# Optimization experiments

Hardware: AMD Instinct MI355X
Metric: run time of the kernel (lower is better)

The kernel has to match this reference:

```python
import jax, jax.numpy as jnp
import numpy as np

ALPHA_MGD = 2e-05
NOISE_SIGMA = 8.0
NOISE_VAR = NOISE_SIGMA ** 2  # 64.0


def _conv2d(x, w, b, pad):
    # x: [N,C,H,W], w: [O,I,kh,kw]
    y = jax.lax.conv_general_dilated(
        x, w, window_strides=(1, 1), padding=[(pad, pad), (pad, pad)],
        dimension_numbers=("NCHW", "OIHW", "NCHW"))
    return y + b[None, :, None, None]


def setup_inputs() -> dict:
    key = jax.random.key(0)
    ks = jax.random.split(key, 8)
    N, Cs, Ct, H, W = 8, 128, 256, 64, 64
    return {
        "preds_S": jax.random.normal(ks[0], (N, Cs, H, W), jnp.float32),
        "preds_T": jax.random.normal(ks[1], (N, Ct, H, W), jnp.float32),
        "W_align": jax.random.normal(ks[2], (Ct, Cs, 1, 1), jnp.float32) * 0.05,
        "b_align": jnp.zeros((Ct,), jnp.float32),
        "W_gen1": jax.random.normal(ks[3], (Ct, Ct, 3, 3), jnp.float32) * 0.02,
        "b_gen1": jnp.zeros((Ct,), jnp.float32),
        "W_gen2": jax.random.normal(ks[4], (Ct, Ct, 3, 3), jnp.float32) * 0.02,
        "b_gen2": jnp.zeros((Ct,), jnp.float32),
    }


def reference(preds_S, preds_T, W_align, b_align, W_gen1, b_gen1, W_gen2, b_gen2):
    # align student channels to teacher channels (1x1 conv)
    s = _conv2d(preds_S, W_align, b_align, pad=0)
    N, C, H, W = preds_T.shape
    # deterministic checkerboard mask: tile([[0,1],[1,0]]) cropped to HxW -> (h+w) % 2
    hh = jnp.arange(H)[:, None]
    ww = jnp.arange(W)[None, :]
    mat = ((hh + ww) % 2).astype(s.dtype)  # [H,W]
    masked_fea = s * mat  # broadcast over [N,C,H,W]
    # generation network: conv3x3 -> relu -> conv3x3
    new_fea = _conv2d(jax.nn.relu(_conv2d(masked_fea, W_gen1, b_gen1, pad=1)), W_gen2, b_gen2, pad=1)
    # bmc_loss_md(pred=preds_T, target=new_fea, noise_var=64):
    # logits[i,j] = MVN(pred_i, noise_var*I).log_prob(target_j); the normalization
    # constant is class-independent and cancels in cross-entropy, keep the quadratic term.
    p = preds_T.reshape(N, -1)   # [N, D], D = C*H*W
    t = new_fea.reshape(N, -1)   # [N, D]
    # pairwise squared L2 via ||p||^2 + ||t||^2 - 2 p.t  (avoids NxNxD blow-up)
    sq = (jnp.sum(p * p, axis=1)[:, None]
          + jnp.sum(t * t, axis=1)[None, :]
          - 2.0 * (p @ t.T))  # [N, N]
    logits = -0.5 * sq / NOISE_VAR
    # cross_entropy(logits, arange(N)) = mean_i (logsumexp_j logits[i,j] - logits[i,i])
    ce = jnp.mean(jax.nn.logsumexp(logits, axis=1) - jnp.diagonal(logits))
    loss = ce * (2.0 * NOISE_VAR) / N
    return loss * ALPHA_MGD
```

## Files before the change

kernel.cpp:

```cpp
#include <hip/hip_runtime.h>

typedef unsigned short u16;
typedef short short8 __attribute__((ext_vector_type(8)));
typedef unsigned short ushort8 __attribute__((ext_vector_type(8)));
typedef float floatx16 __attribute__((ext_vector_type(16)));

#define PLANE8   34848
#define NSTRIDE  1115136

__device__ __forceinline__ u16 f2b(float f) {
  unsigned u = __builtin_bit_cast(unsigned, f);
  return (u16)((u + 0x7FFFu + ((u >> 16) & 1u)) >> 16);
}
__device__ __forceinline__ float b2f(u16 b) {
  return __builtin_bit_cast(float, ((unsigned)b) << 16);
}

typedef const __attribute__((address_space(1))) unsigned int* gptr_t;
typedef __attribute__((address_space(3))) unsigned int* sptr_t;

__global__ __launch_bounds__(256) void kprep(
    const float* __restrict__ Wg1, u16* __restrict__ Wsw1,
    const float* __restrict__ Wg2, u16* __restrict__ Wsw2,
    const float* __restrict__ Wa,  u16* __restrict__ Wb,
    const float* __restrict__ pS,  u16* __restrict__ T,
    u16* __restrict__ masked, u16* __restrict__ t1)
{
  __shared__ u16 Ls[64 * 136];
  int b = blockIdx.x, t = threadIdx.x;

  if (b < 576) {
    const float* W = (b < 288) ? Wg1 : Wg2;
    u16* D = (b < 288) ? Wsw1 : Wsw2;
    int bb = (b < 288) ? b : b - 288;
    int cid = bb * 256 + t;
    int d = cid % 1152, ctcg = cid / 1152;
    int ct = ctcg & 3, cg = ctcg >> 2;
    int colow = d & 31, cihalf = (d >> 5) & 1, sc = (d >> 6) & 1, tap = d >> 7;
    int co = ct * 64 + sc * 32 + colow;
    short8 v;
    #pragma unroll
    for (int jj = 0; jj < 8; ++jj) {
      int ci = cg * 16 + cihalf * 8 + jj;
      v[jj] = (short)f2b(W[((size_t)(co * 256 + ci)) * 9 + tap]);
    }
    *(short8*)&D[(size_t)cid * 8] = v;
  } else if (b < 592) {
    int v = (b - 576) * 256 + t;
    int colow = v & 31, hfb = (v >> 5) & 1, cog = (v >> 6) & 7, k = v >> 9;
    int co = cog * 32 + colow;
    int ci0 = k * 16 + hfb * 8;
    float4 f0 = *(const float4*)(Wa + (size_t)co * 128 + ci0);
    float4 f1 = *(const float4*)(Wa + (size_t)co * 128 + ci0 + 4);
    short8 o;
    o[0] = (short)f2b(f0.x); o[1] = (short)f2b(f0.y);
    o[2] = (short)f2b(f0.z); o[3] = (short)f2b(f0.w);
    o[4] = (short)f2b(f1.x); o[5] = (short)f2b(f1.y);
    o[6] = (short)f2b(f1.z); o[7] = (short)f2b(f1.w);
    *(short8*)&Wb[(size_t)v * 8] = o;
  } else if (b < 1104) {
    int bb = b - 592;
    int n = bb >> 6, pt = bb & 63, pix0 = pt * 64;
    int ci = t >> 1, ph = t & 1;
    const float* src = pS + ((size_t)n * 128 + ci) * 4096 + pix0 + ph * 32;
    #pragma unroll
    for (int i = 0; i < 8; ++i) {
      float4 v4 = *(const float4*)(src + i * 4);
      int pix = ph * 32 + i * 4;
      Ls[(pix + 0) * 136 + ci] = f2b(v4.x);
      Ls[(pix + 1) * 136 + ci] = f2b(v4.y);
      Ls[(pix + 2) * 136 + ci] = f2b(v4.z);
      Ls[(pix + 3) * 136 + ci] = f2b(v4.w);
    }
    __syncthreads();
    int p = t >> 2, q = t & 3;
    const u16* row = Ls + p * 136 + q * 32;
    u16* dst = T + ((size_t)n * 4096 + pix0 + p) * 128 + q * 32;
    #pragma unroll
    for (int k2 = 0; k2 < 4; ++k2)
      *(ushort8*)(dst + k2 * 8) = *(const ushort8*)(row + k2 * 8);
  } else {
    int p = b - 1104;
    u16* base = ((p >> 8) ? t1 : masked);
    int q = p & 255;
    base += (size_t)(q >> 5) * NSTRIDE + (size_t)(q & 31) * PLANE8;
    short8 z;
    #pragma unroll
    for (int jj = 0; jj < 8; ++jj) z[jj] = 0;
    #pragma unroll
    for (int pass = 0; pass < 2; ++pass) {
      int seg = t + pass * 256;
      if (seg < 264) {
        int off;
        if (seg < 66)       off = seg * 8;
        else if (seg < 132) off = (65 * 66 + (seg - 66)) * 8;
        else if (seg < 198) off = ((seg - 132) * 66) * 8;
        else                off = ((seg - 198) * 66 + 65) * 8;
        *(short8*)(base + off) = z;
      }
    }
  }
}

__global__ __launch_bounds__(256) void k1m(const u16* __restrict__ T,
    const u16* __restrict__ Wb, const float* __restrict__ ba,
    u16* __restrict__ mk)
{
  __shared__ __align__(16) u16 Wl[32768];
  int b = blockIdx.x;
  int n = b >> 5, pt = b & 31;
  int t = threadIdx.x, wid = t >> 6, lane = t & 63;
  int ml = lane & 31, hf = lane >> 5;

  #pragma unroll
  for (int kk = 0; kk < 16; ++kk) {
    int chunk = kk * 256 + t;
    __builtin_amdgcn_global_load_lds((gptr_t)(const void*)(Wb + (size_t)chunk * 8),
                                     (sptr_t)(void*)(Wl + chunk * 8), 16, 0, 0);
  }

  const u16* Tn = T + (size_t)n * 524288;
  const u16* ap[4];
  #pragma unroll
  for (int g = 0; g < 4; ++g)
    ap[g] = Tn + (size_t)(pt * 128 + g * 32 + ml) * 128 + hf * 8;

  floatx16 acc[2][4];
  #pragma unroll
  for (int q = 0; q < 2; ++q)
    #pragma unroll
    for (int g = 0; g < 4; ++g)
      #pragma unroll
      for (int i = 0; i < 16; ++i) acc[q][g][i] = 0.f;

  __syncthreads();

  const short8* WlV = (const short8*)Wl;
  int cogb = wid * 2;

  short8 a0[4], a1[4];
  #pragma unroll
  for (int g = 0; g < 4; ++g) a0[g] = *(const short8*)(ap[g]);

#define K1M_STEP(K, CUR, NXT, LAST)                                           \
  {                                                                           \
    if (!(LAST)) {                                                            \
      _Pragma("unroll")                                                       \
      for (int g = 0; g < 4; ++g)                                             \
        NXT[g] = *(const short8*)(ap[g] + ((K) + 1) * 16);                    \
    }                                                                         \
    short8 w0 = WlV[((K) * 8 + cogb) * 64 + lane];                            \
    short8 w1 = WlV[((K) * 8 + cogb + 1) * 64 + lane];                        \
    _Pragma("unroll")                                                         \
    for (int g = 0; g < 4; ++g) {                                             \
      acc[0][g] = __builtin_amdgcn_mfma_f32_32x32x16_bf16(CUR[g], w0, acc[0][g], 0, 0, 0); \
      acc[1][g] = __builtin_amdgcn_mfma_f32_32x32x16_bf16(CUR[g], w1, acc[1][g], 0, 0, 0); \
    }                                                                         \
  }
  K1M_STEP(0, a0, a1, 0)
  K1M_STEP(1, a1, a0, 0)
  K1M_STEP(2, a0, a1, 0)
  K1M_STEP(3, a1, a0, 0)
  K1M_STEP(4, a0, a1, 0)
  K1M_STEP(5, a1, a0, 0)
  K1M_STEP(6, a0, a1, 0)
  K1M_STEP(7, a1, a0, 1)
#undef K1M_STEP

  int co0 = cogb * 32 + ml, co1 = co0 + 32;
  float b0 = ba[co0], b1 = ba[co1];
  u16* base0 = mk + (size_t)n * NSTRIDE + (size_t)(co0 >> 3) * PLANE8 + (co0 & 7);
  u16* base1 = mk + (size_t)n * NSTRIDE + (size_t)(co1 >> 3) * PLANE8 + (co1 & 7);
  #pragma unroll
  for (int g = 0; g < 4; ++g)
    #pragma unroll
    for (int reg = 0; reg < 16; ++reg) {
      int m = (reg & 3) + 8 * (reg >> 2) + 4 * hf;
      int pix = pt * 128 + g * 32 + m;
      int h = pix >> 6, w = pix & 63;
      float msk = (float)((h + w) & 1);
      int off = ((h + 1) * 66 + (w + 1)) * 8;
      base0[off] = f2b((acc[0][g][reg] + b0) * msk);
      base1[off] = f2b((acc[1][g][reg] + b1) * msk);
    }
}

template <int MODE>
__global__ __launch_bounds__(512) void kconv(
    const u16* __restrict__ IN, const u16* __restrict__ WS,
    const float* __restrict__ bg, u16* __restrict__ OUT)
{
  __shared__ __align__(16) u16 L[40960];
  u16* LinA = L;
  u16* LwA  = L + 11264;
  u16* LinB = L + 20480;
  u16* LwB  = L + 31744;

  int b = blockIdx.x;
  int rt = b & 7, ct = (b >> 3) & 3, n = b >> 5;
  int h0 = rt * 8;
  int t = threadIdx.x;
  int wid = t >> 6, lane = t & 63;
  int hf = lane >> 5, ml = lane & 31;

  const u16* inb = IN + (size_t)n * NSTRIDE;
  const u16* wg  = WS + (size_t)ct * 1152 * 8;

  floatx16 acc[2][2];
  #pragma unroll
  for (int s = 0; s < 2; ++s)
    #pragma unroll
    for (int q = 0; q < 2; ++q)
      #pragma unroll
      for (int i = 0; i < 16; ++i) acc[s][q][i] = 0.f;

  auto STAGE = [&](int cg, u16* LinD, u16* LwD) {
    #pragma unroll
    for (int k = 0; k < 3; ++k) {
      int sidx = 8 * k + wid;
      if (sidx < 18) {
        const u16* src = wg + (size_t)cg * 36864 + (size_t)(sidx * 64 + lane) * 8;
        __builtin_amdgcn_global_load_lds((gptr_t)(const void*)src,
                                         (sptr_t)(void*)(LwD + sidx * 512), 16, 0, 0);
      }
    }
    #pragma unroll
    for (int k = 0; k < 3; ++k) {
      int seg = 8 * k + wid;
      if (seg < 22) {
        int half = seg >= 11 ? 1 : 0;
        int s = seg - half * 11;
        const u16* src = inb + (size_t)cg * 69696 + half * PLANE8
                         + (size_t)(h0 * 66 + s * 64 + lane) * 8;
        __builtin_amdgcn_global_load_lds((gptr_t)(const void*)src,
                                         (sptr_t)(void*)(LinD + (half * 704 + s * 64) * 8),
                                         16, 0, 0);
      }
    }
  };

  auto COMPUTE = [&](const u16* LinS, const u16* LwS) {
    const short8* LinV = (const short8*)LinS;
    const short8* LwV  = (const short8*)LwS;
    #pragma unroll
    for (int dr = 0; dr < 3; ++dr) {
      int r0 = hf * 704 + (wid + dr) * 66;
      #pragma unroll
      for (int dc = 0; dc < 3; ++dc) {
        int tap = dr * 3 + dc;
        short8 w0 = LwV[tap * 128 + lane];
        short8 w1 = LwV[tap * 128 + 64 + lane];
        short8 i0 = LinV[r0 + ml + dc];
        short8 i1 = LinV[r0 + 32 + ml + dc];
        acc[0][0] = __builtin_amdgcn_mfma_f32_32x32x16_bf16(i0, w0, acc[0][0], 0, 0, 0);
        acc[0][1] = __builtin_amdgcn_mfma_f32_32x32x16_bf16(i0, w1, acc[0][1], 0, 0, 0);
        acc[1][0] = __builtin_amdgcn_mfma_f32_32x32x16_bf16(i1, w0, acc[1][0], 0, 0, 0);
        acc[1][1] = __builtin_amdgcn_mfma_f32_32x32x16_bf16(i1, w1, acc[1][1], 0, 0, 0);
      }
    }
  };

  STAGE(0, LinA, LwA);
  __syncthreads();
  for (int cg = 0; cg < 16; cg += 2) {
    STAGE(cg + 1, LinB, LwB);
    COMPUTE(LinA, LwA);
    __syncthreads();
    if (cg + 2 < 16) STAGE(cg + 2, LinA, LwA);
    COMPUTE(LinB, LwB);
    __syncthreads();
  }

  float bias0 = bg[ct * 64 + ml];
  float bias1 = bg[ct * 64 + 32 + ml];

  if (MODE == 0) {
    u16* ob = OUT + (size_t)n * NSTRIDE;
    int co0 = ct * 64 + ml, co1 = co0 + 32;
    int cb0 = ((co0 >> 4) * 2 + ((co0 >> 3) & 1)) * PLANE8 + (co0 & 7);
    int cb1 = ((co1 >> 4) * 2 + ((co1 >> 3) & 1)) * PLANE8 + (co1 & 7);
    int rowoff = (h0 + wid + 1) * 66 + 1;
    #pragma unroll
    for (int reg = 0; reg < 16; ++reg) {
      int m = (reg & 3) + 8 * (reg >> 2) + 4 * hf;
      float v;
      v = acc[0][0][reg] + bias0; v = fmaxf(v, 0.f); ob[cb0 + (rowoff + m) * 8] = f2b(v);
      v = acc[0][1][reg] + bias1; v = fmaxf(v, 0.f); ob[cb1 + (rowoff + m) * 8] = f2b(v);
      v = acc[1][0][reg] + bias0; v = fmaxf(v, 0.f); ob[cb0 + (rowoff + 32 + m) * 8] = f2b(v);
      v = acc[1][1][reg] + bias1; v = fmaxf(v, 0.f); ob[cb1 + (rowoff + 32 + m) * 8] = f2b(v);
    }
  } else {
    u16* plane = L + wid * 4352;
    #pragma unroll
    for (int reg = 0; reg < 16; ++reg) {
      int m = (reg & 3) + 8 * (reg >> 2) + 4 * hf;
      plane[ml * 68 + m]              = f2b(acc[0][0][reg] + bias0);
      plane[(32 + ml) * 68 + m]       = f2b(acc[0][1][reg] + bias1);
      plane[ml * 68 + 32 + m]         = f2b(acc[1][0][reg] + bias0);
      plane[(32 + ml) * 68 + 32 + m]  = f2b(acc[1][1][reg] + bias1);
    }
    const u16* row = plane + lane * 68;
    __align__(16) u16 tmp[64];
    #pragma unroll
    for (int k2 = 0; k2 < 16; ++k2)
      *(ushort4*)(tmp + k2 * 4) = *(const ushort4*)(row + k2 * 4);
    u16* gdst = OUT + (size_t)n * 1048576 + (size_t)(ct * 64 + lane) * 4096
                + (h0 + wid) * 64;
    #pragma unroll
    for (int k2 = 0; k2 < 8; ++k2)
      *(ushort8*)(gdst + k2 * 8) = *(const ushort8*)(tmp + k2 * 8);
  }
}

__global__ __launch_bounds__(256) void kbmc(const u16* __restrict__ t2,
    const float* __restrict__ pT, float* __restrict__ part)
{
  int t = threadIdx.x, lane = t & 63, role = t >> 6;
  int ih = role >> 1, nh = role & 1;
  int bid = blockIdx.x;

  float pt[4][4], pp[4], tt[4];
  #pragma unroll
  for (int i = 0; i < 4; ++i) {
    pp[i] = 0.f; tt[i] = 0.f;
    #pragma unroll
    for (int j = 0; j < 4; ++j) pt[i][j] = 0.f;
  }

  const float* pb = pT + ((size_t)ih * 4) * 1048576;
  const u16*   tb = t2 + ((size_t)nh * 4) * 1048576;

  for (int k = 0; k < 8; ++k) {
    size_t d0 = ((size_t)(bid * 512 + k * 64 + lane)) * 4;
    float4 p[4], tf[4];
    #pragma unroll
    for (int i = 0; i < 4; ++i)
      p[i] = *(const float4*)(pb + (size_t)i * 1048576 + d0);
    #pragma unroll
    for (int j = 0; j < 4; ++j) {
      ushort4 tv = *(const ushort4*)(tb + (size_t)j * 1048576 + d0);
      tf[j] = make_float4(b2f(tv.x), b2f(tv.y), b2f(tv.z), b2f(tv.w));
    }
    if (nh == 0) {
      #pragma unroll
      for (int i = 0; i < 4; ++i)
        pp[i] += p[i].x * p[i].x + p[i].y * p[i].y + p[i].z * p[i].z + p[i].w * p[i].w;
    }
    if (ih == 0) {
      #pragma unroll
      for (int j = 0; j < 4; ++j)
        tt[j] += tf[j].x * tf[j].x + tf[j].y * tf[j].y + tf[j].z * tf[j].z + tf[j].w * tf[j].w;
    }
    #pragma unroll
    for (int i = 0; i < 4; ++i)
      #pragma unroll
      for (int j = 0; j < 4; ++j)
        pt[i][j] += p[i].x * tf[j].x + p[i].y * tf[j].y
                  + p[i].z * tf[j].z + p[i].w * tf[j].w;
  }

  #pragma unroll
  for (int m = 1; m < 64; m <<= 1) {
    #pragma unroll
    for (int i = 0; i < 4; ++i) {
      pp[i] += __shfl_xor(pp[i], m);
      tt[i] += __shfl_xor(tt[i], m);
      #pragma unroll
      for (int j = 0; j < 4; ++j) pt[i][j] += __shfl_xor(pt[i][j], m);
    }
  }
  if (lane == 0) {
    #pragma unroll
    for (int i = 0; i < 4; ++i)
      #pragma unroll
      for (int j = 0; j < 4; ++j)
        part[(size_t)(16 + (ih * 4 + i) * 8 + (nh * 4 + j)) * 512 + bid] = pt[i][j];
    if (nh == 0) {
      #pragma unroll
      for (int i = 0; i < 4; ++i) part[(size_t)(ih * 4 + i) * 512 + bid] = pp[i];
    }
    if (ih == 0) {
      #pragma unroll
      for (int j = 0; j < 4; ++j) part[(size_t)(8 + nh * 4 + j) * 512 + bid] = tt[j];
    }
  }
}

__global__ __launch_bounds__(256) void kred(const float* __restrict__ part,
                                            float* __restrict__ accums)
{
  __shared__ float r4[4];
  int s = blockIdx.x, t = threadIdx.x, lane = t & 63, wid = t >> 6;
  float v = part[(size_t)s * 512 + t] + part[(size_t)s * 512 + 256 + t];
  #pragma unroll
  for (int m = 1; m < 64; m <<= 1) v += __shfl_xor(v, m);
  if (lane == 0) r4[wid] = v;
  __syncthreads();
  if (t == 0) accums[s] = r4[0] + r4[1] + r4[2] + r4[3];
}

__global__ void k4_final(const float* __restrict__ accums, float* __restrict__ out)
{
  int t = threadIdx.x;
  int i = t >> 3, j = t & 7;
  double pp = accums[i];
  double tt = accums[8 + j];
  double pt = accums[16 + i * 8 + j];
  double logit = -0.5 * (pp + tt - 2.0 * pt) / 64.0;
  double m = logit;
  #pragma unroll
  for (int s = 1; s < 8; s <<= 1) {
    double o = __shfl_xor(m, s);
    m = o > m ? o : m;
  }
  double e = exp(logit - m);
  #pragma unroll
  for (int s = 1; s < 8; s <<= 1) e += __shfl_xor(e, s);
  double lse = m + log(e);
  double term = (j == i) ? (lse - logit) : 0.0;
  #pragma unroll
  for (int s = 1; s < 64; s <<= 1) term += __shfl_xor(term, s);
  if (t == 0) {
    double ce = term / 8.0;
    out[0] = (float)(ce * (2.0 * 64.0) / 8.0 * 2e-05);
  }
}

extern "C" void kernel_launch(void* const* d_in, const int* in_sizes, int n_in,
                              void* d_out, int out_size, void* d_ws, size_t ws_size,
                              hipStream_t stream)
{
  const float* preds_S = (const float*)d_in[0];
  const float* preds_T = (const float*)d_in[1];
  const float* W_align = (const float*)d_in[2];
  const float* b_align = (const float*)d_in[3];
  const float* W_gen1  = (const float*)d_in[4];
  const float* b_gen1  = (const float*)d_in[5];
  const float* W_gen2  = (const float*)d_in[6];
  const float* b_gen2  = (const float*)d_in[7];
  float* out = (float*)d_out;

  char* wsb = (char*)d_ws;
  u16* masked = (u16*)wsb;
  u16* t1     = (u16*)(wsb + 17842176);
  u16* t2p    = (u16*)(wsb + 35684352);
  u16* T      = t2p;
  u16* Wsw1   = (u16*)(wsb + 52461568);
  u16* Wsw2   = (u16*)(wsb + 53641216);
  float* part   = (float*)(wsb + 54820864);
  float* accums = (float*)(wsb + 55017472);
  u16* Wb     = (u16*)(wsb + 55017856);

  kprep<<<1616, 256, 0, stream>>>(W_gen1, Wsw1, W_gen2, Wsw2, W_align, Wb,
                                  preds_S, T, masked, t1);
  k1m<<<256, 256, 0, stream>>>(T, Wb, b_align, masked);
  kconv<0><<<256, 512, 0, stream>>>(masked, Wsw1, b_gen1, t1);
  kconv<1><<<256, 512, 0, stream>>>(t1, Wsw2, b_gen2, t2p);
  kbmc<<<512, 256, 0, stream>>>(t2p, preds_T, part);
  kred<<<80, 256, 0, stream>>>(part, accums);
  k4_final<<<1, 64, 0, stream>>>(accums, out);
}
```

Baseline: 208.0 us.

## Store checkerboard-masked features compactly and skip zero taps in first 3x3 conv

The aligned student features are now stored in a compacted layout that holds only the nonzero checkerboard pixels, roughly halving the masked buffer. A new conv kernel (kconvs) for the first generator conv exploits the parity structure: for each output parity only the taps that hit nonzero inputs are computed (4 or 5 of the 9). This removes about half of the MFMA work and input traffic for that conv. In exchange it adds parity-dependent indexing and a new padding layout that must exactly match the zeroing in kprep and the writes in k1m.

```diff
diff --git a/kernel.cpp b/kernel.cpp
--- a/kernel.cpp
+++ b/kernel.cpp
@@ -5,6 +5,8 @@
 typedef unsigned short ushort8 __attribute__((ext_vector_type(8)));
 typedef float floatx16 __attribute__((ext_vector_type(16)));
 
+#define PLANE8C  17952
+#define NSTRIDEC 574464
 #define PLANE8   34848
 #define NSTRIDE  1115136
 
@@ -24,7 +26,7 @@
     const float* __restrict__ Wg2, u16* __restrict__ Wsw2,
     const float* __restrict__ Wa,  u16* __restrict__ Wb,
     const float* __restrict__ pS,  u16* __restrict__ T,
-    u16* __restrict__ masked, u16* __restrict__ t1)
+    u16* __restrict__ maskedC, u16* __restrict__ t1)
 {
   __shared__ u16 Ls[64 * 136];
   int b = blockIdx.x, t = threadIdx.x;
@@ -79,11 +81,23 @@
     #pragma unroll
     for (int k2 = 0; k2 < 4; ++k2)
       *(ushort8*)(dst + k2 * 8) = *(const ushort8*)(row + k2 * 8);
+  } else if (b < 1360) {
+    int p = b - 1104;
+    u16* base = maskedC + (size_t)(p >> 5) * NSTRIDEC + (size_t)(p & 31) * PLANE8C;
+    short8 z;
+    #pragma unroll
+    for (int jj = 0; jj < 8; ++jj) z[jj] = 0;
+    if (t < 200) {
+      int off;
+      if (t < 34)       off = t * 8;
+      else if (t < 68)  off = (65 * 34 + (t - 34)) * 8;
+      else if (t < 134) off = ((t - 68) * 34) * 8;
+      else              off = ((t - 134) * 34 + 33) * 8;
+      *(short8*)(base + off) = z;
+    }
   } else {
-    int p = b - 1104;
-    u16* base = ((p >> 8) ? t1 : masked);
-    int q = p & 255;
-    base += (size_t)(q >> 5) * NSTRIDE + (size_t)(q & 31) * PLANE8;
+    int p = b - 1360;
+    u16* base = t1 + (size_t)(p >> 5) * NSTRIDE + (size_t)(p & 31) * PLANE8;
     short8 z;
     #pragma unroll
     for (int jj = 0; jj < 8; ++jj) z[jj] = 0;
@@ -169,8 +183,8 @@
 
   int co0 = cogb * 32 + ml, co1 = co0 + 32;
   float b0 = ba[co0], b1 = ba[co1];
-  u16* base0 = mk + (size_t)n * NSTRIDE + (size_t)(co0 >> 3) * PLANE8 + (co0 & 7);
-  u16* base1 = mk + (size_t)n * NSTRIDE + (size_t)(co1 >> 3) * PLANE8 + (co1 & 7);
+  u16* base0 = mk + (size_t)n * NSTRIDEC + (size_t)(co0 >> 3) * PLANE8C + (co0 & 7);
+  u16* base1 = mk + (size_t)n * NSTRIDEC + (size_t)(co1 >> 3) * PLANE8C + (co1 & 7);
   #pragma unroll
   for (int g = 0; g < 4; ++g)
     #pragma unroll
@@ -178,11 +192,132 @@
       int m = (reg & 3) + 8 * (reg >> 2) + 4 * hf;
       int pix = pt * 128 + g * 32 + m;
       int h = pix >> 6, w = pix & 63;
-      float msk = (float)((h + w) & 1);
-      int off = ((h + 1) * 66 + (w + 1)) * 8;
-      base0[off] = f2b((acc[0][g][reg] + b0) * msk);
-      base1[off] = f2b((acc[1][g][reg] + b1) * msk);
-    }
+      if (((h + w) & 1) == 1) {
+        int j = (w - ((h + 1) & 1)) >> 1;
+        int off = ((h + 1) * 34 + 1 + j) * 8;
+        base0[off] = f2b(acc[0][g][reg] + b0);
+        base1[off] = f2b(acc[1][g][reg] + b1);
+      }
+    }
+}
+
+__global__ __launch_bounds__(512) void kconvs(
+    const u16* __restrict__ IN, const u16* __restrict__ WS,
+    const float* __restrict__ bg, u16* __restrict__ OUT)
+{
+  __shared__ __align__(16) u16 L[30720];
+  u16* LinA = L;
+  u16* LwA  = L + 6144;
+  u16* LinB = L + 15360;
+  u16* LwB  = L + 21504;
+
+  int b = blockIdx.x;
+  int rt = b & 7, ct = (b >> 3) & 3, n = b >> 5;
+  int h0 = rt * 8;
+  int t = threadIdx.x;
+  int wid = t >> 6, lane = t & 63;
+  int hf = lane >> 5, ml = lane & 31;
+  int e = wid & 1;
+
+  const u16* inb = IN + (size_t)n * NSTRIDEC;
+  const u16* wg  = WS + (size_t)ct * 1152 * 8;
+
+  floatx16 acc[2][2];
+  #pragma unroll
+  for (int p = 0; p < 2; ++p)
+    #pragma unroll
+    for (int q = 0; q < 2; ++q)
+      #pragma unroll
+      for (int i = 0; i < 16; ++i) acc[p][q][i] = 0.f;
+
+  auto STAGE = [&](int cg, u16* LinD, u16* LwD) {
+    #pragma unroll
+    for (int k = 0; k < 4; ++k) {
+      int seg = wid + 8 * k;
+      if (seg < 18) {
+        const u16* src = wg + (size_t)cg * 36864 + (size_t)(seg * 64 + lane) * 8;
+        __builtin_amdgcn_global_load_lds((gptr_t)(const void*)src,
+                                         (sptr_t)(void*)(LwD + seg * 512), 16, 0, 0);
+      } else if (seg < 30) {
+        int ii = seg - 18;
+        int hh = ii >= 6 ? 1 : 0;
+        int s = ii - hh * 6;
+        const u16* src = inb + (size_t)cg * (2 * PLANE8C) + (size_t)hh * PLANE8C
+                         + (size_t)(h0 * 34 + s * 64 + lane) * 8;
+        __builtin_amdgcn_global_load_lds((gptr_t)(const void*)src,
+                                         (sptr_t)(void*)(LinD + (hh * 384 + s * 64) * 8),
+                                         16, 0, 0);
+      }
+    }
+  };
+
+  auto COMPUTE = [&](const u16* LinS, const u16* LwS) {
+    const short8* LinV = (const short8*)LinS;
+    const short8* LwV  = (const short8*)LwS;
+    int rA = hf * 384 + wid * 34 + 1 + ml;
+    int rS = rA + 34;
+    int rB = rA + 68;
+    short8 iA0 = LinV[rA];
+    short8 iS0 = LinV[rS];
+    short8 iB0 = LinV[rB];
+    short8 iSm = LinV[rS + e - 1];
+    short8 iSp = LinV[rS + e];
+    short8 iAm = LinV[rA - e];
+    short8 iAp = LinV[rA + 1 - e];
+    short8 iBm = LinV[rB - e];
+    short8 iBp = LinV[rB + 1 - e];
+    #pragma unroll
+    for (int q = 0; q < 2; ++q) {
+      short8 w0 = LwV[0 * 128 + q * 64 + lane];
+      short8 w1 = LwV[1 * 128 + q * 64 + lane];
+      short8 w2 = LwV[2 * 128 + q * 64 + lane];
+      short8 w3 = LwV[3 * 128 + q * 64 + lane];
+      short8 w4 = LwV[4 * 128 + q * 64 + lane];
+      short8 w5 = LwV[5 * 128 + q * 64 + lane];
+      short8 w6 = LwV[6 * 128 + q * 64 + lane];
+      short8 w7 = LwV[7 * 128 + q * 64 + lane];
+      short8 w8 = LwV[8 * 128 + q * 64 + lane];
+      acc[0][q] = __builtin_amdgcn_mfma_f32_32x32x16_bf16(iA0, w1, acc[0][q], 0, 0, 0);
+      acc[0][q] = __builtin_amdgcn_mfma_f32_32x32x16_bf16(iSm, w3, acc[0][q], 0, 0, 0);
+      acc[0][q] = __builtin_amdgcn_mfma_f32_32x32x16_bf16(iSp, w5, acc[0][q], 0, 0, 0);
+      acc[0][q] = __builtin_amdgcn_mfma_f32_32x32x16_bf16(iB0, w7, acc[0][q], 0, 0, 0);
+      acc[1][q] = __builtin_amdgcn_mfma_f32_32x32x16_bf16(iAm, w0, acc[1][q], 0, 0, 0);
+      acc[1][q] = __builtin_amdgcn_mfma_f32_32x32x16_bf16(iAp, w2, acc[1][q], 0, 0, 0);
+      acc[1][q] = __builtin_amdgcn_mfma_f32_32x32x16_bf16(iS0, w4, acc[1][q], 0, 0, 0);
+      acc[1][q] = __builtin_amdgcn_mfma_f32_32x32x16_bf16(iBm, w6, acc[1][q], 0, 0, 0);
+      acc[1][q] = __builtin_amdgcn_mfma_f32_32x32x16_bf16(iBp, w8, acc[1][q], 0, 0, 0);
+    }
+  };
+
+  STAGE(0, LinA, LwA);
+  __syncthreads();
+  for (int cg = 0; cg < 16; cg += 2) {
+    STAGE(cg + 1, LinB, LwB);
+    COMPUTE(LinA, LwA);
+    __syncthreads();
+    if (cg + 2 < 16) STAGE(cg + 2, LinA, LwA);
+    COMPUTE(LinB, LwB);
+    __syncthreads();
+  }
+
+  float bias0 = bg[ct * 64 + ml];
+  float bias1 = bg[ct * 64 + 32 + ml];
+
+  u16* ob = OUT + (size_t)n * NSTRIDE;
+  int co0 = ct * 64 + ml, co1 = co0 + 32;
+  int cb0 = ((co0 >> 4) * 2 + ((co0 >> 3) & 1)) * PLANE8 + (co0 & 7);
+  int cb1 = ((co1 >> 4) * 2 + ((co1 >> 3) & 1)) * PLANE8 + (co1 & 7);
+  int rowoff = (h0 + wid + 1) * 66 + 1;
+  #pragma unroll
+  for (int reg = 0; reg < 16; ++reg) {
+    int m = (reg & 3) + 8 * (reg >> 2) + 4 * hf;
+    int we = 2 * m + e, wo = 2 * m + 1 - e;
+    float v;
+    v = acc[0][0][reg] + bias0; v = fmaxf(v, 0.f); ob[cb0 + (rowoff + we) * 8] = f2b(v);
+    v = acc[0][1][reg] + bias1; v = fmaxf(v, 0.f); ob[cb1 + (rowoff + we) * 8] = f2b(v);
+    v = acc[1][0][reg] + bias0; v = fmaxf(v, 0.f); ob[cb0 + (rowoff + wo) * 8] = f2b(v);
+    v = acc[1][1][reg] + bias1; v = fmaxf(v, 0.f); ob[cb1 + (rowoff + wo) * 8] = f2b(v);
+  }
 }
 
 template <int MODE>
@@ -441,20 +576,20 @@
   float* out = (float*)d_out;
 
   char* wsb = (char*)d_ws;
-  u16* masked = (u16*)wsb;
-  u16* t1     = (u16*)(wsb + 17842176);
-  u16* t2p    = (u16*)(wsb + 35684352);
+  u16* maskedC = (u16*)wsb;
+  u16* t1     = (u16*)(wsb + 9191424);
+  u16* t2p    = (u16*)(wsb + 27033600);
   u16* T      = t2p;
-  u16* Wsw1   = (u16*)(wsb + 52461568);
-  u16* Wsw2   = (u16*)(wsb + 53641216);
-  float* part   = (float*)(wsb + 54820864);
-  float* accums = (float*)(wsb + 55017472);
-  u16* Wb     = (u16*)(wsb + 55017856);
+  u16* Wsw1   = (u16*)(wsb + 43810816);
+  u16* Wsw2   = (u16*)(wsb + 44990464);
+  float* part   = (float*)(wsb + 46170112);
+  float* accums = (float*)(wsb + 46366720);
+  u16* Wb     = (u16*)(wsb + 46367104);
 
   kprep<<<1616, 256, 0, stream>>>(W_gen1, Wsw1, W_gen2, Wsw2, W_align, Wb,
-                                  preds_S, T, masked, t1);
-  k1m<<<256, 256, 0, stream>>>(T, Wb, b_align, masked);
-  kconv<0><<<256, 512, 0, stream>>>(masked, Wsw1, b_gen1, t1);
+                                  preds_S, T, maskedC, t1);
+  k1m<<<256, 256, 0, stream>>>(T, Wb, b_align, maskedC);
+  kconvs<<<256, 512, 0, stream>>>(maskedC, Wsw1, b_gen1, t1);
   kconv<1><<<256, 512, 0, stream>>>(t1, Wsw2, b_gen2, t2p);
   kbmc<<<512, 256, 0, stream>>>(t2p, preds_T, part);
   kred<<<80, 256, 0, stream>>>(part, accums);
```

New measurement: 192.7 us (median of 2 runs). 7.4% less time.
